# Kernel tuning notes

Measured on AMD Instinct MI355X. Metric: run time of the kernel, lower is better.

The kernel has to match this reference:

```python
import jax, jax.numpy as jnp
import numpy as np

B, N, E = 128, 2048, 32768   # events, nodes per history graph, temporal edges per graph
C, TC, H = 4, 4, 2           # channels, time_channels, heads (hardcoded in source)
DH = C // H
L = 2                        # num_layers


def setup_inputs() -> dict:
    key = jax.random.key(0)
    ks = jax.random.split(key, 16)
    return {
        "x": jax.random.normal(ks[0], (B, N, C), jnp.float32),
        "edge_index": jax.random.randint(ks[1], (B, 2, E), 0, N),
        "edge_time": jax.random.uniform(ks[2], (B, E), jnp.float32),
        "timestamp": jax.random.uniform(ks[3], (B,), jnp.float32),
        "src_index": jax.random.randint(ks[4], (B,), 0, N),
        "dst_index": jax.random.randint(ks[5], (B,), 0, N),
        "time_w": jax.random.normal(ks[6], (TC,), jnp.float32),
        "time_b": jax.random.normal(ks[7], (TC,), jnp.float32),
        "Wq": jax.random.normal(ks[8], (L, C, C), jnp.float32) / np.sqrt(C).astype(np.float32),
        "Wk": jax.random.normal(ks[9], (L, C + TC, C), jnp.float32) / np.sqrt(C + TC).astype(np.float32),
        "Wv": jax.random.normal(ks[10], (L, C + TC, C), jnp.float32) / np.sqrt(C + TC).astype(np.float32),
        "Wo": jax.random.normal(ks[11], (L, C, C), jnp.float32) / np.sqrt(C).astype(np.float32),
        "bo": jnp.zeros((L, C), jnp.float32),
        "W_lin": jax.random.normal(ks[12], (2 * C + TC, 2), jnp.float32) / np.sqrt(2 * C + TC).astype(np.float32),
        "b_lin": jnp.zeros((2,), jnp.float32),
    }


def _time_enc(t, w, b):
    # TimeEncoder: cos(t * w + b)  (Bochner-style functional time encoding)
    return jnp.cos(t[..., None] * w + b)


def _encode(x, src, dst, phi, Wq, Wk, Wv, Wo, bo):
    # seg id per edge: (batch, dst node) -> flat segment for segment softmax
    seg = (jnp.arange(B, dtype=dst.dtype)[:, None] * N + dst).reshape(-1)  # [B*E]
    h = x
    for l in range(L):
        h_src = jnp.take_along_axis(h, src[:, :, None], axis=1)            # [B,E,C] gather source feats
        msg = jnp.concatenate([h_src, phi], axis=-1)                       # [B,E,C+TC]
        q = (h @ Wq[l]).reshape(B, N, C)                                   # [B,N,C]
        k = (msg @ Wk[l]).reshape(B, E, H, DH)
        v = (msg @ Wv[l]).reshape(B, E, H, DH)
        q_e = jnp.take_along_axis(q, dst[:, :, None], axis=1).reshape(B, E, H, DH)
        logits = (q_e * k).sum(-1) / np.float32(np.sqrt(DH))               # [B,E,H]
        lf = logits.reshape(B * E, H)
        m = jax.ops.segment_max(lf, seg, num_segments=B * N)               # stable softmax max
        p = jnp.exp(lf - m[seg])
        s = jax.ops.segment_sum(p, seg, num_segments=B * N)
        agg = jax.ops.segment_sum(p[:, :, None] * v.reshape(B * E, H, DH), seg, num_segments=B * N)
        attn = (agg / jnp.where(s == 0, 1.0, s)[:, :, None]).reshape(B, N, C)
        h = jax.nn.relu(h + attn @ Wo[l] + bo[l])                          # residual + out-proj + relu
    return h


def reference(x, edge_index, edge_time, timestamp, src_index, dst_index,
              time_w, time_b, Wq, Wk, Wv, Wo, bo, W_lin, b_lin):
    src, dst = edge_index[:, 0, :], edge_index[:, 1, :]
    dt = timestamp[:, None] - edge_time                                    # [B,E] time deltas vs query time
    phi = _time_enc(dt, time_w, time_b)                                    # [B,E,TC]
    h = _encode(x, src, dst, phi, Wq, Wk, Wv, Wo, bo)                      # [B,N,C]
    bidx = jnp.arange(B)
    src_x = h[bidx, src_index]                                             # [B,C]
    dst_x = h[bidx, dst_index]                                             # [B,C]
    time_x = _time_enc(timestamp, time_w, time_b)                          # [B,TC]
    feats = jnp.concatenate([src_x, dst_x, time_x], axis=-1)               # [B,12]
    return feats @ W_lin + b_lin                                           # [B,2]
```

## Files before the change

kernel.cpp:

```cpp
#include <hip/hip_runtime.h>

namespace {

constexpr int B = 128, N = 2048, E = 32768;
constexpr int LOG2N = 11, LOG2E = 15;
constexpr int QE = E / 4;
constexpr int LOG2QE = 13;

constexpr size_t OFF_H0 = 0;
constexpr size_t OFF_H1 = 4u * 1024 * 1024;
constexpr size_t OFF_S8 = 8u * 1024 * 1024;
constexpr size_t OFF_RP = 40u * 1024 * 1024;

__global__ __launch_bounds__(1024) void sort_kernel(const int* __restrict__ edge_index,
                                                    const float* __restrict__ edge_time,
                                                    const float* __restrict__ timestamp,
                                                    int2* __restrict__ sorted8,
                                                    int* __restrict__ row_ptr) {
  __shared__ int  cnt[N];
  __shared__ int  wsum[16];
  __shared__ int2 rec[QE];
  int blk = blockIdx.x, b = blk >> 2, q = blk & 3, t = threadIdx.x;

  cnt[t] = 0; cnt[t + 1024] = 0;
  __syncthreads();

  const int* src_arr = edge_index + (((size_t)(2 * b)) << LOG2E) + q * QE;
  const int* dst_arr = edge_index + (((size_t)(2 * b + 1)) << LOG2E) + q * QE;
  const float* et    = edge_time + (((size_t)b) << LOG2E) + q * QE;
  float ts = timestamp[b];

  int srcv[8], dstv[8]; float dtv[8];
#pragma unroll
  for (int k = 0; k < 8; ++k) {
    int e = t + k * 1024;
    srcv[k] = src_arr[e];
    dstv[k] = dst_arr[e];
    dtv[k]  = ts - et[e];
  }

#pragma unroll
  for (int k = 0; k < 8; ++k) atomicAdd(&cnt[dstv[k]], 1);
  __syncthreads();

  int i0 = 2 * t, i1 = 2 * t + 1;
  int l0 = cnt[i0], l1 = cnt[i1];
  int sum = l0 + l1;
  int lane = t & 63, wid = t >> 6;
  int incl = sum;
#pragma unroll
  for (int d = 1; d < 64; d <<= 1) {
    int v = __shfl_up(incl, d, 64);
    if (lane >= d) incl += v;
  }
  if (lane == 63) wsum[wid] = incl;
  __syncthreads();
  if (t < 16) {
    int v = wsum[t];
    int inc = v;
#pragma unroll
    for (int d = 1; d < 16; d <<= 1) {
      int u = __shfl_up(inc, d, 16);
      if (t >= d) inc += u;
    }
    wsum[t] = inc - v;
  }
  __syncthreads();
  int run = wsum[wid] + (incl - sum);
  int run2 = run + l0;
  int* rp = row_ptr + (size_t)blk * (N + 1);
  rp[i0] = run;
  rp[i1] = run2;
  if (t == 1023) rp[N] = QE;
  cnt[i0] = run;
  cnt[i1] = run2;
  __syncthreads();

#pragma unroll
  for (int k = 0; k < 8; ++k) {
    int pos = atomicAdd(&cnt[dstv[k]], 1);
    rec[pos] = make_int2(srcv[k], __float_as_int(dtv[k]));
  }
  __syncthreads();

  const int4* rec4 = (const int4*)rec;
  int4* out4 = (int4*)(sorted8 + (((size_t)blk) << LOG2QE));
#pragma unroll
  for (int i = t; i < QE / 2; i += 1024) out4[i] = rec4[i];
}

__global__ __launch_bounds__(1024) void layer_kernel(const float4* __restrict__ h_in,
                                                     float4* __restrict__ h_out,
                                                     const int* __restrict__ row_ptr,
                                                     const int2* __restrict__ sorted8,
                                                     const float* __restrict__ tw,
                                                     const float* __restrict__ tb,
                                                     const float* __restrict__ Wq,
                                                     const float* __restrict__ Wk,
                                                     const float* __restrict__ Wv,
                                                     const float* __restrict__ Wo,
                                                     const float* __restrict__ bo) {
  __shared__ float4 lh[N];
  int blk = blockIdx.x, b = blk >> 1, half = blk & 1, t = threadIdx.x;

  const float4* hb = h_in + (((size_t)b) << LOG2N);
  lh[t] = hb[t];
  lh[t + 1024] = hb[t + 1024];

  constexpr float INV2PI = 0.15915494309189535f;
  constexpr float QSCALE = 0.70710678118654752f * 1.4426950408889634f;
  float twf2[4], tbf2[4], wq[16], wkh[16], wkp[16], wvh[16], wvp[16];
#pragma unroll
  for (int j = 0; j < 4; j++) { twf2[j] = tw[j] * INV2PI; tbf2[j] = tb[j] * INV2PI; }
#pragma unroll
  for (int j = 0; j < 16; j++) wq[j] = Wq[j];
#pragma unroll
  for (int j = 0; j < 16; j++) { wkh[j] = Wk[j]; wkp[j] = Wk[16 + j]; }
#pragma unroll
  for (int j = 0; j < 16; j++) { wvh[j] = Wv[j]; wvp[j] = Wv[16 + j]; }
  __syncthreads();

  int n = half * 1024 + t;
  {
    float4 hn = lh[n];
    float q0 = (hn.x * wq[0] + hn.y * wq[4] + hn.z * wq[8]  + hn.w * wq[12]) * QSCALE;
    float q1 = (hn.x * wq[1] + hn.y * wq[5] + hn.z * wq[9]  + hn.w * wq[13]) * QSCALE;
    float q2 = (hn.x * wq[2] + hn.y * wq[6] + hn.z * wq[10] + hn.w * wq[14]) * QSCALE;
    float q3 = (hn.x * wq[3] + hn.y * wq[7] + hn.z * wq[11] + hn.w * wq[15]) * QSCALE;
#pragma unroll
    for (int i = 0; i < 4; i++) {
      wq[i]      = q0 * wkh[i * 4 + 0] + q1 * wkh[i * 4 + 1];
      wq[4 + i]  = q2 * wkh[i * 4 + 2] + q3 * wkh[i * 4 + 3];
      wq[8 + i]  = q0 * wkp[i * 4 + 0] + q1 * wkp[i * 4 + 1];
      wq[12 + i] = q2 * wkp[i * 4 + 2] + q3 * wkp[i * 4 + 3];
    }
  }

  int stage = 0, addr, rem, total;
  int b1, b2, b3, c1, c2, c3;
  {
    const int* rp0 = row_ptr + (size_t)(b * 4 + 0) * (N + 1);
    const int* rp1 = row_ptr + (size_t)(b * 4 + 1) * (N + 1);
    const int* rp2 = row_ptr + (size_t)(b * 4 + 2) * (N + 1);
    const int* rp3 = row_ptr + (size_t)(b * 4 + 3) * (N + 1);
    int s0 = rp0[n], e0 = rp0[n + 1];
    int s1 = rp1[n], e1 = rp1[n + 1];
    int s2 = rp2[n], e2 = rp2[n + 1];
    int s3 = rp3[n], e3 = rp3[n + 1];
    int c0 = e0 - s0; c1 = e1 - s1; c2 = e2 - s2; c3 = e3 - s3;
    total = c0 + c1 + c2 + c3;
    addr = ((b * 4 + 0) << LOG2QE) + s0; rem = c0;
    b1 = ((b * 4 + 1) << LOG2QE) + s1;
    b2 = ((b * 4 + 2) << LOG2QE) + s2;
    b3 = ((b * 4 + 3) << LOG2QE) + s3;
    while (rem <= 0 && stage < 3) {
      ++stage;
      addr = (stage == 1) ? b1 : (stage == 2) ? b2 : b3;
      rem  = (stage == 1) ? c1 : (stage == 2) ? c2 : c3;
    }
  }

#define ADV() do { ++addr; --rem;                                   \
    while (rem <= 0 && stage < 3) { ++stage;                        \
      addr = (stage == 1) ? b1 : (stage == 2) ? b2 : b3;            \
      rem  = (stage == 1) ? c1 : (stage == 2) ? c2 : c3; } } while (0)
#define HW_COS(d, s) asm("v_cos_f32 %0, %1" : "=v"(d) : "v"(s))
#define HW_EXP2(d, s) asm("v_exp_f32 %0, %1" : "=v"(d) : "v"(s))

  float s0v = 0.f, s1v = 0.f, a00 = 0.f, a01 = 0.f, a10 = 0.f, a11 = 0.f;

  int2 r0 = sorted8[addr]; ADV();
  int2 r1 = sorted8[addr]; ADV();
  int2 r2 = sorted8[addr]; ADV();
  int2 r3 = sorted8[addr]; ADV();
  float4 hsN = lh[r0.x & (N - 1)];

  for (int it = 0; it < total; ++it) {
    int2 cur = r0;
    float4 hs = hsN;
    r0 = r1; r1 = r2; r2 = r3;
    r3 = sorted8[addr]; ADV();
    hsN = lh[r0.x & (N - 1)];

    float dt = __int_as_float(cur.y);
    float ph0, ph1, ph2, ph3;
    HW_COS(ph0, dt * twf2[0] + tbf2[0]);
    HW_COS(ph1, dt * twf2[1] + tbf2[1]);
    HW_COS(ph2, dt * twf2[2] + tbf2[2]);
    HW_COS(ph3, dt * twf2[3] + tbf2[3]);

    float l0 = hs.x * wq[0] + hs.y * wq[1] + hs.z * wq[2]  + hs.w * wq[3]
             + ph0 * wq[8] + ph1 * wq[9] + ph2 * wq[10] + ph3 * wq[11];
    float l1 = hs.x * wq[4] + hs.y * wq[5] + hs.z * wq[6]  + hs.w * wq[7]
             + ph0 * wq[12] + ph1 * wq[13] + ph2 * wq[14] + ph3 * wq[15];

    float p0, p1;
    HW_EXP2(p0, l0);
    HW_EXP2(p1, l1);

    float v0 = hs.x * wvh[0] + hs.y * wvh[4] + hs.z * wvh[8]  + hs.w * wvh[12]
             + ph0 * wvp[0] + ph1 * wvp[4] + ph2 * wvp[8]  + ph3 * wvp[12];
    float v1 = hs.x * wvh[1] + hs.y * wvh[5] + hs.z * wvh[9]  + hs.w * wvh[13]
             + ph0 * wvp[1] + ph1 * wvp[5] + ph2 * wvp[9]  + ph3 * wvp[13];
    float v2 = hs.x * wvh[2] + hs.y * wvh[6] + hs.z * wvh[10] + hs.w * wvh[14]
             + ph0 * wvp[2] + ph1 * wvp[6] + ph2 * wvp[10] + ph3 * wvp[14];
    float v3 = hs.x * wvh[3] + hs.y * wvh[7] + hs.z * wvh[11] + hs.w * wvh[15]
             + ph0 * wvp[3] + ph1 * wvp[7] + ph2 * wvp[11] + ph3 * wvp[15];

    s0v += p0; a00 += p0 * v0; a01 += p0 * v1;
    s1v += p1; a10 += p1 * v2; a11 += p1 * v3;
  }
#undef ADV
#undef HW_COS
#undef HW_EXP2

  float den0 = (s0v == 0.f) ? 1.f : s0v;
  float den1 = (s1v == 0.f) ? 1.f : s1v;
  float at0 = a00 / den0, at1 = a01 / den0, at2 = a10 / den1, at3 = a11 / den1;

  float wof[16], bof[4];
#pragma unroll
  for (int j = 0; j < 16; j++) wof[j] = Wo[j];
#pragma unroll
  for (int j = 0; j < 4; j++) bof[j] = bo[j];

  float4 hn = lh[n];
  float o0 = bof[0] + at0 * wof[0] + at1 * wof[4] + at2 * wof[8]  + at3 * wof[12];
  float o1 = bof[1] + at0 * wof[1] + at1 * wof[5] + at2 * wof[9]  + at3 * wof[13];
  float o2 = bof[2] + at0 * wof[2] + at1 * wof[6] + at2 * wof[10] + at3 * wof[14];
  float o3 = bof[3] + at0 * wof[3] + at1 * wof[7] + at2 * wof[11] + at3 * wof[15];
  h_out[(((size_t)b) << LOG2N) + n] =
      make_float4(fmaxf(hn.x + o0, 0.f), fmaxf(hn.y + o1, 0.f),
                  fmaxf(hn.z + o2, 0.f), fmaxf(hn.w + o3, 0.f));
}

__global__ void final_kernel(const float4* __restrict__ h,
                             const int* __restrict__ src_index, const int* __restrict__ dst_index,
                             const float* __restrict__ timestamp,
                             const float* __restrict__ tw,
                             const float* __restrict__ tb,
                             const float* __restrict__ W_lin,
                             const float* __restrict__ b_lin,
                             float* __restrict__ out) {
  int b = threadIdx.x;
  if (b >= B) return;
  float4 sx = h[(((size_t)b) << LOG2N) + src_index[b]];
  float4 dx = h[(((size_t)b) << LOG2N) + dst_index[b]];
  float ts = timestamp[b];
  float f[12];
  f[0] = sx.x; f[1] = sx.y; f[2] = sx.z; f[3] = sx.w;
  f[4] = dx.x; f[5] = dx.y; f[6] = dx.z; f[7] = dx.w;
#pragma unroll
  for (int j = 0; j < 4; j++) f[8 + j] = __cosf(ts * tw[j] + tb[j]);
#pragma unroll
  for (int c = 0; c < 2; c++) {
    float o = b_lin[c];
#pragma unroll
    for (int j = 0; j < 12; j++) o += f[j] * W_lin[j * 2 + c];
    out[b * 2 + c] = o;
  }
}

}

extern "C" void kernel_launch(void* const* d_in, const int* in_sizes, int n_in,
                              void* d_out, int out_size, void* d_ws, size_t ws_size,
                              hipStream_t stream) {
  (void)in_sizes; (void)n_in; (void)out_size; (void)ws_size;
  const float* x         = (const float*)d_in[0];
  const int*   edge_idx  = (const int*)d_in[1];
  const float* edge_time = (const float*)d_in[2];
  const float* timestamp = (const float*)d_in[3];
  const int*   src_index = (const int*)d_in[4];
  const int*   dst_index = (const int*)d_in[5];
  const float* time_w    = (const float*)d_in[6];
  const float* time_b    = (const float*)d_in[7];
  const float* Wq        = (const float*)d_in[8];
  const float* Wk        = (const float*)d_in[9];
  const float* Wv        = (const float*)d_in[10];
  const float* Wo        = (const float*)d_in[11];
  const float* bo        = (const float*)d_in[12];
  const float* W_lin     = (const float*)d_in[13];
  const float* b_lin     = (const float*)d_in[14];

  char* ws = (char*)d_ws;
  float4* h0      = (float4*)(ws + OFF_H0);
  float4* h1      = (float4*)(ws + OFF_H1);
  int2*   sorted8 = (int2*)(ws + OFF_S8);
  int*    row_ptr = (int*)(ws + OFF_RP);

  sort_kernel<<<4 * B, 1024, 0, stream>>>(edge_idx, edge_time, timestamp, sorted8, row_ptr);

  layer_kernel<<<2 * B, 1024, 0, stream>>>((const float4*)x, h1, row_ptr, sorted8,
                                           time_w, time_b,
                                           Wq + 0 * 16, Wk + 0 * 32, Wv + 0 * 32,
                                           Wo + 0 * 16, bo + 0 * 4);
  layer_kernel<<<2 * B, 1024, 0, stream>>>(h1, h0, row_ptr, sorted8,
                                           time_w, time_b,
                                           Wq + 1 * 16, Wk + 1 * 32, Wv + 1 * 32,
                                           Wo + 1 * 16, bo + 1 * 4);

  final_kernel<<<1, 128, 0, stream>>>(h0, src_index, dst_index, timestamp, time_w, time_b,
                                      W_lin, b_lin, (float*)d_out);
}
```

Baseline: 166.7 us.

## Split each node's edge walk across two threads and merge partials in shared memory

The layer kernel now launches four blocks per graph instead of two. Each node gets two threads, and each thread walks the edges from two of the four sorted quarter-lists instead of all four. The partial softmax sums and weighted accumulators are merged through a shared-memory buffer before the output projection, and the launch bounds now request 4 blocks per CU. This aims to shorten the serial per-thread edge loop and raise parallelism, at the cost of an extra barrier and shared-memory merge, with half the threads idle during the epilogue.

After: 175.0 us. +5.0%, slower.

```diff
diff --git a/kernel.cpp b/kernel.cpp
--- a/kernel.cpp
+++ b/kernel.cpp
@@ -89,19 +89,21 @@
   for (int i = t; i < QE / 2; i += 1024) out4[i] = rec4[i];
 }
 
-__global__ __launch_bounds__(1024) void layer_kernel(const float4* __restrict__ h_in,
-                                                     float4* __restrict__ h_out,
-                                                     const int* __restrict__ row_ptr,
-                                                     const int2* __restrict__ sorted8,
-                                                     const float* __restrict__ tw,
-                                                     const float* __restrict__ tb,
-                                                     const float* __restrict__ Wq,
-                                                     const float* __restrict__ Wk,
-                                                     const float* __restrict__ Wv,
-                                                     const float* __restrict__ Wo,
-                                                     const float* __restrict__ bo) {
+__global__ __launch_bounds__(1024, 4) void layer_kernel(const float4* __restrict__ h_in,
+                                                        float4* __restrict__ h_out,
+                                                        const int* __restrict__ row_ptr,
+                                                        const int2* __restrict__ sorted8,
+                                                        const float* __restrict__ tw,
+                                                        const float* __restrict__ tb,
+                                                        const float* __restrict__ Wq,
+                                                        const float* __restrict__ Wk,
+                                                        const float* __restrict__ Wv,
+                                                        const float* __restrict__ Wo,
+                                                        const float* __restrict__ bo) {
   __shared__ float4 lh[N];
-  int blk = blockIdx.x, b = blk >> 1, half = blk & 1, t = threadIdx.x;
+  __shared__ float  mrg[512 * 7];
+  int blk = blockIdx.x, b = blk >> 2, nq = blk & 3, t = threadIdx.x;
+  int nloc = t & 511, kpair = t >> 9;
 
   const float4* hb = h_in + (((size_t)b) << LOG2N);
   lh[t] = hb[t];
@@ -120,7 +122,7 @@
   for (int j = 0; j < 16; j++) { wvh[j] = Wv[j]; wvp[j] = Wv[16 + j]; }
   __syncthreads();
 
-  int n = half * 1024 + t;
+  int n = nq * 512 + nloc;
   {
     float4 hn = lh[n];
     float q0 = (hn.x * wq[0] + hn.y * wq[4] + hn.z * wq[8]  + hn.w * wq[12]) * QSCALE;
@@ -136,34 +138,21 @@
     }
   }
 
-  int stage = 0, addr, rem, total;
-  int b1, b2, b3, c1, c2, c3;
+  int qA = b * 4 + 2 * kpair, qB = qA + 1;
+  int addr, rem, total, addrB, cB;
   {
-    const int* rp0 = row_ptr + (size_t)(b * 4 + 0) * (N + 1);
-    const int* rp1 = row_ptr + (size_t)(b * 4 + 1) * (N + 1);
-    const int* rp2 = row_ptr + (size_t)(b * 4 + 2) * (N + 1);
-    const int* rp3 = row_ptr + (size_t)(b * 4 + 3) * (N + 1);
-    int s0 = rp0[n], e0 = rp0[n + 1];
-    int s1 = rp1[n], e1 = rp1[n + 1];
-    int s2 = rp2[n], e2 = rp2[n + 1];
-    int s3 = rp3[n], e3 = rp3[n + 1];
-    int c0 = e0 - s0; c1 = e1 - s1; c2 = e2 - s2; c3 = e3 - s3;
-    total = c0 + c1 + c2 + c3;
-    addr = ((b * 4 + 0) << LOG2QE) + s0; rem = c0;
-    b1 = ((b * 4 + 1) << LOG2QE) + s1;
-    b2 = ((b * 4 + 2) << LOG2QE) + s2;
-    b3 = ((b * 4 + 3) << LOG2QE) + s3;
-    while (rem <= 0 && stage < 3) {
-      ++stage;
-      addr = (stage == 1) ? b1 : (stage == 2) ? b2 : b3;
-      rem  = (stage == 1) ? c1 : (stage == 2) ? c2 : c3;
-    }
-  }
-
-#define ADV() do { ++addr; --rem;                                   \
-    while (rem <= 0 && stage < 3) { ++stage;                        \
-      addr = (stage == 1) ? b1 : (stage == 2) ? b2 : b3;            \
-      rem  = (stage == 1) ? c1 : (stage == 2) ? c2 : c3; } } while (0)
+    const int* rpA = row_ptr + (size_t)qA * (N + 1);
+    const int* rpB = row_ptr + (size_t)qB * (N + 1);
+    int sA = rpA[n], cA = rpA[n + 1] - sA;
+    int sB = rpB[n]; cB = rpB[n + 1] - sB;
+    total = cA + cB;
+    addr  = (qA << LOG2QE) + sA; rem = cA;
+    addrB = (qB << LOG2QE) + sB;
+    if (rem <= 0) { addr = addrB; rem = cB; cB = -1; }
+  }
+
+#define ADV() do { ++addr; --rem;                                     \
+    if (rem <= 0 && cB >= 0) { addr = addrB; rem = cB; cB = -1; } } while (0)
 #define HW_COS(d, s) asm("v_cos_f32 %0, %1" : "=v"(d) : "v"(s))
 #define HW_EXP2(d, s) asm("v_exp_f32 %0, %1" : "=v"(d) : "v"(s))
 
@@ -214,24 +203,38 @@
 #undef HW_COS
 #undef HW_EXP2
 
-  float den0 = (s0v == 0.f) ? 1.f : s0v;
-  float den1 = (s1v == 0.f) ? 1.f : s1v;
-  float at0 = a00 / den0, at1 = a01 / den0, at2 = a10 / den1, at3 = a11 / den1;
-
-  float wof[16], bof[4];
-#pragma unroll
-  for (int j = 0; j < 16; j++) wof[j] = Wo[j];
-#pragma unroll
-  for (int j = 0; j < 4; j++) bof[j] = bo[j];
-
-  float4 hn = lh[n];
-  float o0 = bof[0] + at0 * wof[0] + at1 * wof[4] + at2 * wof[8]  + at3 * wof[12];
-  float o1 = bof[1] + at0 * wof[1] + at1 * wof[5] + at2 * wof[9]  + at3 * wof[13];
-  float o2 = bof[2] + at0 * wof[2] + at1 * wof[6] + at2 * wof[10] + at3 * wof[14];
-  float o3 = bof[3] + at0 * wof[3] + at1 * wof[7] + at2 * wof[11] + at3 * wof[15];
-  h_out[(((size_t)b) << LOG2N) + n] =
-      make_float4(fmaxf(hn.x + o0, 0.f), fmaxf(hn.y + o1, 0.f),
-                  fmaxf(hn.z + o2, 0.f), fmaxf(hn.w + o3, 0.f));
+  if (kpair) {
+    int base = nloc * 7;
+    mrg[base + 0] = s0v; mrg[base + 1] = s1v;
+    mrg[base + 2] = a00; mrg[base + 3] = a01;
+    mrg[base + 4] = a10; mrg[base + 5] = a11;
+  }
+  __syncthreads();
+  if (!kpair) {
+    int base = nloc * 7;
+    s0v += mrg[base + 0]; s1v += mrg[base + 1];
+    a00 += mrg[base + 2]; a01 += mrg[base + 3];
+    a10 += mrg[base + 4]; a11 += mrg[base + 5];
+
+    float den0 = (s0v == 0.f) ? 1.f : s0v;
+    float den1 = (s1v == 0.f) ? 1.f : s1v;
+    float at0 = a00 / den0, at1 = a01 / den0, at2 = a10 / den1, at3 = a11 / den1;
+
+    float wof[16], bof[4];
+#pragma unroll
+    for (int j = 0; j < 16; j++) wof[j] = Wo[j];
+#pragma unroll
+    for (int j = 0; j < 4; j++) bof[j] = bo[j];
+
+    float4 hn = lh[n];
+    float o0 = bof[0] + at0 * wof[0] + at1 * wof[4] + at2 * wof[8]  + at3 * wof[12];
+    float o1 = bof[1] + at0 * wof[1] + at1 * wof[5] + at2 * wof[9]  + at3 * wof[13];
+    float o2 = bof[2] + at0 * wof[2] + at1 * wof[6] + at2 * wof[10] + at3 * wof[14];
+    float o3 = bof[3] + at0 * wof[3] + at1 * wof[7] + at2 * wof[11] + at3 * wof[15];
+    h_out[(((size_t)b) << LOG2N) + n] =
+        make_float4(fmaxf(hn.x + o0, 0.f), fmaxf(hn.y + o1, 0.f),
+                    fmaxf(hn.z + o2, 0.f), fmaxf(hn.w + o3, 0.f));
+  }
 }
 
 __global__ void final_kernel(const float4* __restrict__ h,
@@ -291,11 +294,11 @@
 
   sort_kernel<<<4 * B, 1024, 0, stream>>>(edge_idx, edge_time, timestamp, sorted8, row_ptr);
 
-  layer_kernel<<<2 * B, 1024, 0, stream>>>((const float4*)x, h1, row_ptr, sorted8,
+  layer_kernel<<<4 * B, 1024, 0, stream>>>((const float4*)x, h1, row_ptr, sorted8,
                                            time_w, time_b,
                                            Wq + 0 * 16, Wk + 0 * 32, Wv + 0 * 32,
                                            Wo + 0 * 16, bo + 0 * 4);
-  layer_kernel<<<2 * B, 1024, 0, stream>>>(h1, h0, row_ptr, sorted8,
+  layer_kernel<<<4 * B, 1024, 0, stream>>>(h1, h0, row_ptr, sorted8,
                                            time_w, time_b,
                                            Wq + 1 * 16, Wk + 1 * 32, Wv + 1 * 32,
                                            Wo + 1 * 16, bo + 1 * 4);
```
